# Optimization experiments

Measured on AMD Instinct MI355X. Metric: run time of the kernel, lower is better.

Reference implementation:

```python
import jax, jax.numpy as jnp
import numpy as np

INCH, OUTCH, H, W = 1536, 256, 60, 60
B = 4


def resize_bilinear_align_corners(x, oh, ow):
    """F.interpolate(x, (oh, ow), mode='bilinear', align_corners=True) for NCHW x."""
    Bx, C, Hx, Wx = x.shape
    ys = jnp.linspace(0.0, Hx - 1.0, oh)
    xs = jnp.linspace(0.0, Wx - 1.0, ow)
    y0 = jnp.floor(ys).astype(jnp.int32)
    x0 = jnp.floor(xs).astype(jnp.int32)
    y1 = jnp.minimum(y0 + 1, Hx - 1)
    x1 = jnp.minimum(x0 + 1, Wx - 1)
    wy = (ys - y0.astype(x.dtype))[:, None]   # [oh,1]
    wx = (xs - x0.astype(x.dtype))[None, :]   # [1,ow]
    g = lambda yi, xi: x[:, :, yi][:, :, :, xi]  # [B,C,oh,ow]
    top = (1.0 - wx) * g(y0, x0) + wx * g(y0, x1)
    bot = (1.0 - wx) * g(y1, x0) + wx * g(y1, x1)
    return (1.0 - wy) * top + wy * bot


def setup_inputs() -> dict:
    key = jax.random.key(0)
    ks = jax.random.split(key, 8)
    feat_supp = jax.random.normal(ks[0], (B, INCH, H, W), dtype=jnp.float32)
    feat_query = jax.random.normal(ks[1], (B, INCH, H, W), dtype=jnp.float32)
    mask_supp = jax.random.uniform(ks[2], (B, 1, 473, 473), dtype=jnp.float32)
    scale = 0.02
    W_lpf = jax.random.normal(ks[3], (OUTCH, INCH), dtype=jnp.float32) * scale   # shared_LPF 1x1 conv
    W_supp = jax.random.normal(ks[4], (OUTCH, INCH), dtype=jnp.float32) * scale  # supp_linear
    W_query = jax.random.normal(ks[5], (OUTCH, INCH), dtype=jnp.float32) * scale # query_linear
    W_final = jax.random.normal(ks[6], (OUTCH, 2 * OUTCH), dtype=jnp.float32) * scale
    b_final = jax.random.normal(ks[7], (OUTCH,), dtype=jnp.float32) * scale
    return {"feat_supp": feat_supp, "feat_query": feat_query, "mask_supp": mask_supp,
            "W_lpf": W_lpf, "W_supp": W_supp, "W_query": W_query,
            "W_final": W_final, "b_final": b_final}


def conv1x1(x, Wm):
    # x: [b,c,h,w], Wm: [o,c]
    return jnp.einsum('bchw,oc->bohw', x, Wm)


def reference(feat_supp, feat_query, mask_supp, W_lpf, W_supp, W_query, W_final, b_final):
    b, d, h, w = feat_supp.shape
    hw = h * w
    v_supp = conv1x1(feat_supp, W_lpf)    # [b,256,h,w]
    v_query = conv1x1(feat_query, W_lpf)  # [b,256,h,w]
    k = conv1x1(feat_supp, W_supp).transpose(0, 2, 3, 1).reshape(b, hw, -1)   # [b,hw,256]
    q = conv1x1(feat_query, W_query).transpose(0, 2, 3, 1).reshape(b, hw, -1) # [b,hw,256]
    attn = jnp.einsum('bqd,bkd->bqk', q, k)  # [b,hw,hw]
    fg_mask = resize_bilinear_align_corners(mask_supp, h, w)  # [b,1,h,w]
    bg_suppress = ((1.0 - fg_mask) * -999.0).reshape(b, 1, hw)
    attn = jax.nn.softmax(attn + bg_suppress, axis=-1)
    vs = v_supp.transpose(0, 2, 3, 1).reshape(b, hw, -1)      # [b,hw,256]
    out = jnp.einsum('bqk,bkd->bqd', attn, vs)                # [b,hw,256]
    out = out.reshape(b, h, w, -1).transpose(0, 3, 1, 2)      # [b,256,h,w]
    cat = jnp.concatenate([out, v_query], axis=1)             # [b,512,h,w]
    final = jax.nn.relu(conv1x1(cat, W_final) + b_final[None, :, None, None])
    return final, attn.reshape(b, h, w, h, w)
```

## Files before the change

### kernel.cpp

```cpp
#include <hip/hip_runtime.h>
#include <stdint.h>

typedef unsigned short u16;
typedef _Float16 h16;
typedef __attribute__((ext_vector_type(4))) float f32x4;
typedef __attribute__((ext_vector_type(8))) short s16x8;
typedef __attribute__((ext_vector_type(8))) _Float16 h16x8;
typedef __attribute__((ext_vector_type(4))) _Float16 h16x4;
typedef __attribute__((ext_vector_type(4))) unsigned short u16x4;
typedef __attribute__((ext_vector_type(8))) unsigned short u16x8;

#define HW   3600
#define HWP  3648
#define DIM  256
#define CIN  1536
#define LDK  72
#define NCB  58
#define PSH  15.0f

__device__ __forceinline__ u16 f2bf(float f) {
  uint32_t u = __float_as_uint(f);
  uint32_t r = (u + 0x7fffu + ((u >> 16) & 1u)) >> 16;
  return (u16)r;
}
__device__ __forceinline__ float bf2f(u16 h) { return __uint_as_float((uint32_t)h << 16); }

template<int MR, int NR>
__device__ __forceinline__ void mfma_tile(const h16 (*As)[LDK], const h16 (*Bs)[LDK],
                                          int lane, int wr, int wc, f32x4 acc[MR][NR]) {
#pragma unroll
  for (int ks = 0; ks < 2; ++ks) {
    const int ko = ks * 32 + ((lane >> 4) << 3);
    h16x8 af[MR], bv[NR];
#pragma unroll
    for (int m = 0; m < MR; ++m) af[m] = *(const h16x8*)&As[wr + m * 16 + (lane & 15)][ko];
#pragma unroll
    for (int n = 0; n < NR; ++n) bv[n] = *(const h16x8*)&Bs[wc + n * 16 + (lane & 15)][ko];
#pragma unroll
    for (int m = 0; m < MR; ++m)
#pragma unroll
      for (int n = 0; n < NR; ++n)
        acc[m][n] = __builtin_amdgcn_mfma_f32_16x16x32_f16(af[m], bv[n], acc[m][n], 0, 0, 0);
  }
}

template<int MR, int NR>
__device__ __forceinline__ void mfma_tile_bf(const u16 (*As)[LDK], const u16 (*Bs)[LDK],
                                             int lane, int wr, int wc, f32x4 acc[MR][NR]) {
#pragma unroll
  for (int ks = 0; ks < 2; ++ks) {
    const int ko = ks * 32 + ((lane >> 4) << 3);
    s16x8 af[MR], bv[NR];
#pragma unroll
    for (int m = 0; m < MR; ++m) af[m] = *(const s16x8*)&As[wr + m * 16 + (lane & 15)][ko];
#pragma unroll
    for (int n = 0; n < NR; ++n) bv[n] = *(const s16x8*)&Bs[wc + n * 16 + (lane & 15)][ko];
#pragma unroll
    for (int m = 0; m < MR; ++m)
#pragma unroll
      for (int n = 0; n < NR; ++n)
        acc[m][n] = __builtin_amdgcn_mfma_f32_16x16x32_bf16(af[m], bv[n], acc[m][n], 0, 0, 0);
  }
}

#define NW    (256 * 1536)
#define NWF   (256 * 512)
#define NPAD  (4 * 256 * 48)
#define NPREP (14400 + 3 * NW + NWF + NPAD)

__global__ __launch_bounds__(256) void k_prep(
    const float* __restrict__ mask, const float* __restrict__ Wlpf,
    const float* __restrict__ Wsupp, const float* __restrict__ Wquery,
    const float* __restrict__ Wfin,
    float* __restrict__ sup, h16* __restrict__ Wl16, h16* __restrict__ Ws16,
    h16* __restrict__ Wq16, h16* __restrict__ Wf16, u16* __restrict__ vs) {
  int i = blockIdx.x * 256 + threadIdx.x;
  if (i < 14400) {
    int b = i / HW, p = i % HW, py = p / 60, px = p % 60;
    float fg = mask[(size_t)b * 473 * 473 + (size_t)(py * 8) * 473 + px * 8];
    sup[i] = (1.0f - fg) * -999.0f;
  } else if (i < 14400 + NW) {
    int j = i - 14400; Wl16[j] = (h16)Wlpf[j];
  } else if (i < 14400 + 2 * NW) {
    int j = i - 14400 - NW; Ws16[j] = (h16)Wsupp[j];
  } else if (i < 14400 + 3 * NW) {
    int j = i - 14400 - 2 * NW; Wq16[j] = (h16)Wquery[j];
  } else if (i < 14400 + 3 * NW + NWF) {
    int j = i - 14400 - 3 * NW; Wf16[j] = (h16)Wfin[j];
  } else if (i < NPREP) {
    int j = i - 14400 - 3 * NW - NWF;
    int b = j / (256 * 48), rem = j % (256 * 48), d = rem / 48, kk = rem % 48;
    vs[((size_t)b * DIM + d) * HWP + 3600 + kk] = 0;
  }
}

__global__ __launch_bounds__(512, 4) void k_conv(
    const h16* __restrict__ Wl16, const h16* __restrict__ Ws16, const h16* __restrict__ Wq16,
    const float* __restrict__ featS, const float* __restrict__ featQ,
    u16* __restrict__ vs, h16* __restrict__ vq,
    h16* __restrict__ kbuf, h16* __restrict__ qbuf) {
  const int lin = blockIdx.x;
  const int xcd = lin & 7, slot = lin >> 3;
  const int ct = slot >> 1, rb = slot & 1;
  const int b = xcd & 3, isQ = xcd >> 2;
  const int colBase = ct * 128;
  const int tid = threadIdx.x, lane = tid & 63, wid = tid >> 6;
  const int wr = (wid >> 1) << 6, wc = (wid & 1) << 6;
  const h16* Wsel = (rb == 0) ? Wl16 : (isQ ? Wq16 : Ws16);
  const float* feat = (isQ ? featQ : featS) + (size_t)b * CIN * HW;

  __shared__ h16 As[256][LDK];
  __shared__ h16 Bs[128][LDK];
  f32x4 acc[4][4] = {};

  const int a_r = tid >> 3, a_kv = (tid & 7) << 3;
  const int b_px = (tid & 31) << 2;
  const int b_kb = (tid >> 5) << 2;
  const int gpx0 = colBase + b_px;
  const int gpx = (gpx0 + 3 < HW) ? gpx0 : HW - 4;

  s16x8 aR[4];
  f32x4 bV[4];
#pragma unroll
  for (int i = 0; i < 4; ++i)
    aR[i] = *(const s16x8*)&Wsel[(size_t)(a_r + i * 64) * CIN + a_kv];
#pragma unroll
  for (int i = 0; i < 4; ++i)
    bV[i] = *(const f32x4*)&feat[(size_t)(b_kb + i) * HW + gpx];

  for (int kt = 0; kt < 24; ++kt) {
#pragma unroll
    for (int i = 0; i < 4; ++i) *(s16x8*)&As[a_r + i * 64][a_kv] = aR[i];
#pragma unroll
    for (int c = 0; c < 4; ++c) {
      h16x4 h = {(h16)bV[0][c], (h16)bV[1][c], (h16)bV[2][c], (h16)bV[3][c]};
      *(h16x4*)&Bs[b_px + c][b_kb] = h;
    }
    if (kt < 23) {
      const int k0n = (kt + 1) * 64;
#pragma unroll
      for (int i = 0; i < 4; ++i)
        aR[i] = *(const s16x8*)&Wsel[(size_t)(a_r + i * 64) * CIN + k0n + a_kv];
#pragma unroll
      for (int i = 0; i < 4; ++i)
        bV[i] = *(const f32x4*)&feat[(size_t)(k0n + b_kb + i) * HW + gpx];
    }
    __syncthreads();
    mfma_tile<4, 4>(As, Bs, lane, wr, wc, acc);
    __syncthreads();
  }

  if (rb == 0 && !isQ) {
    u16* dst = vs + (size_t)b * DIM * HWP;
#pragma unroll
    for (int m = 0; m < 4; ++m) {
      const int d0 = wr + m * 16 + ((lane >> 4) << 2);
#pragma unroll
      for (int n = 0; n < 4; ++n) {
        const int pix = colBase + wc + n * 16 + (lane & 15);
        if (pix < HW) {
#pragma unroll
          for (int r = 0; r < 4; ++r) dst[(size_t)(d0 + r) * HWP + pix] = f2bf(acc[m][n][r]);
        }
      }
    }
  } else {
    h16* dst = ((rb == 0) ? vq : (isQ ? qbuf : kbuf)) + (size_t)b * HW * DIM;
#pragma unroll
    for (int m = 0; m < 4; ++m) {
      const int d0 = wr + m * 16 + ((lane >> 4) << 2);
#pragma unroll
      for (int n = 0; n < 4; ++n) {
        const int pix = colBase + wc + n * 16 + (lane & 15);
        if (pix < HW) {
          h16x4 h = {(h16)acc[m][n][0], (h16)acc[m][n][1],
                     (h16)acc[m][n][2], (h16)acc[m][n][3]};
          *(h16x4*)&dst[(size_t)pix * DIM + d0] = h;
        }
      }
    }
  }
}

__global__ __launch_bounds__(256) void k_qk(
    const h16* __restrict__ qbuf, const h16* __restrict__ kbuf,
    const float* __restrict__ sup, u16* __restrict__ p, float* __restrict__ stat) {
  const int hwid = blockIdx.x;
  const int xcd = hwid & 7, pos = hwid >> 3;
  const int logical = (xcd < 4) ? xcd * 421 + pos : 1684 + (xcd - 4) * 420 + pos;
  const int b = logical / 841, rem = logical % 841;
  const int rt = rem / 29, ct = rem % 29;
  const int rowBase = rt * 128, colBase = ct * 128;
  const int tid = threadIdx.x, lane = tid & 63, wid = tid >> 6;
  const int wr = (wid >> 1) << 6, wc = (wid & 1) << 6;
  const h16* Aq = qbuf + (size_t)b * HW * DIM;
  const h16* Bk = kbuf + (size_t)b * HW * DIM;

  __shared__ __align__(16) char smem[128 * LDK * 2 * 2];
  h16 (*As)[LDK] = (h16(*)[LDK])smem;
  h16 (*Bs)[LDK] = (h16(*)[LDK])(smem + 128 * LDK * 2);
  u16 (*pC)[136] = (u16(*)[136])smem;

  f32x4 acc[4][4] = {};
  const int r0 = tid >> 3, kv8 = (tid & 7) << 3;

  int gaR[4], gbR[4];
#pragma unroll
  for (int i = 0; i < 4; ++i) {
    const int r = r0 + i * 32;
    int ga = rowBase + r; gaR[i] = ga < HW ? ga : HW - 1;
    int gb = colBase + r; gbR[i] = gb < HW ? gb : HW - 1;
  }
  s16x8 aR[4], bR[4];
#pragma unroll
  for (int i = 0; i < 4; ++i) {
    aR[i] = *(const s16x8*)(Aq + (size_t)gaR[i] * DIM + kv8);
    bR[i] = *(const s16x8*)(Bk + (size_t)gbR[i] * DIM + kv8);
  }

  for (int kt = 0; kt < 4; ++kt) {
#pragma unroll
    for (int i = 0; i < 4; ++i) {
      *(s16x8*)&As[r0 + i * 32][kv8] = aR[i];
      *(s16x8*)&Bs[r0 + i * 32][kv8] = bR[i];
    }
    if (kt < 3) {
      const int k0n = (kt + 1) * 64;
#pragma unroll
      for (int i = 0; i < 4; ++i) {
        aR[i] = *(const s16x8*)(Aq + (size_t)gaR[i] * DIM + k0n + kv8);
        bR[i] = *(const s16x8*)(Bk + (size_t)gbR[i] * DIM + k0n + kv8);
      }
    }
    __syncthreads();
    mfma_tile<4, 4>(As, Bs, lane, wr, wc, acc);
    __syncthreads();
  }

  float sup4[4]; int kp4[4];
#pragma unroll
  for (int n = 0; n < 4; ++n) {
    const int kp = colBase + wc + n * 16 + (lane & 15);
    kp4[n] = kp;
    sup4[n] = (kp < HW) ? sup[b * HW + kp] : 0.f;
  }
  float* st = stat + (size_t)(b * NCB + ct * 2 + (wc >> 6)) * HW;
#pragma unroll
  for (int m = 0; m < 4; ++m) {
#pragma unroll
    for (int r = 0; r < 4; ++r) {
      float pr[4];
      float ls = 0.f;
#pragma unroll
      for (int n = 0; n < 4; ++n) {
        pr[n] = (kp4[n] < HW) ? __expf(acc[m][n][r] + sup4[n] - PSH) : 0.f;
        ls += pr[n];
      }
#pragma unroll
      for (int off = 1; off < 16; off <<= 1) ls += __shfl_xor(ls, off);
      const int rl = wr + m * 16 + ((lane >> 4) << 2) + r;
      if ((lane & 15) == 0) {
        const int qp = rowBase + rl;
        if (qp < HW) st[qp] = ls;
      }
#pragma unroll
      for (int n = 0; n < 4; ++n) pC[rl][wc + n * 16 + (lane & 15)] = f2bf(pr[n]);
    }
  }
  __syncthreads();
  u16* pB = p + (size_t)b * HW * HWP;
#pragma unroll
  for (int pass = 0; pass < 8; ++pass) {
    const int rl = pass * 16 + (tid >> 4);
    const int qp = rowBase + rl;
    const int col = colBase + (tid & 15) * 8;
    if (qp < HW && col < HW) {
      u16x8 v = *(const u16x8*)&pC[rl][(tid & 15) * 8];
      *(u16x8*)&pB[(size_t)qp * HWP + col] = v;
    }
  }
}

__global__ __launch_bounds__(256) void k_rowsum(const float* __restrict__ stat,
                                                float* __restrict__ invS) {
  const int i = blockIdx.x * 256 + threadIdx.x;
  if (i >= 4 * HW) return;
  const int b = i / HW, row = i % HW;
  const float* s = stat + (size_t)b * NCB * HW + row;
  float S = 0.f;
  for (int c = 0; c < NCB; ++c) S += s[(size_t)c * HW];
  invS[i] = 1.0f / S;
}

__global__ __launch_bounds__(256) void k_pvsm(
    const u16* __restrict__ p, const u16* __restrict__ vs,
    const float* __restrict__ invS, float* __restrict__ attn, float* __restrict__ part) {
  const int lin = blockIdx.x;
  const int xcd = lin & 7, slot = lin >> 3;
  const int b = xcd >> 1, sphalf = xcd & 1;
  const int split = sphalf * 2 + (slot & 1);
  const int rt = slot >> 1;
  const int rowBase = rt * 64;
  const int tid = threadIdx.x, lane = tid & 63, wid = tid >> 6;
  const int wc = wid << 6;
  const u16* pB = p + (size_t)b * HW * HWP;
  const u16* Bv = vs + (size_t)b * DIM * HWP;
  float* Ab = attn + (size_t)b * HW * HW;

  __shared__ u16 As[64][LDK];
  __shared__ u16 Bs[256][LDK];
  __shared__ float Ir[64];
  f32x4 acc[4][4] = {};

  if (tid < 64) {
    const int ga = rowBase + tid;
    Ir[tid] = (ga < HW) ? invS[b * HW + ga] : 0.f;
  }
  __syncthreads();

  const int a_r = tid >> 4, a_kv = (tid & 15) << 2;
  const int b_r = tid >> 3, b_kv = (tid & 7) << 3;
  const int t0 = split * 15, t1 = (split == 3) ? 57 : split * 15 + 15;

  u16x4 pR[4];
  s16x8 vR[8];
  {
    const int kc = t0 * 64 + a_kv;
#pragma unroll
    for (int i = 0; i < 4; ++i) {
      const int ga = rowBase + a_r + i * 16;
      pR[i] = (u16x4){0, 0, 0, 0};
      if (ga < HW && kc < HW) pR[i] = *(const u16x4*)&pB[(size_t)ga * HWP + kc];
    }
#pragma unroll
    for (int i = 0; i < 8; ++i)
      vR[i] = *(const s16x8*)&Bv[(size_t)(b_r + i * 32) * HWP + t0 * 64 + b_kv];
  }

  for (int kt = t0; kt < t1; ++kt) {
    const int kc = kt * 64 + a_kv;
#pragma unroll
    for (int i = 0; i < 4; ++i) {
      const int r = a_r + i * 16;
      const int ga = rowBase + r;
      if (ga < HW && kc < HW) {
        const float I = Ir[r];
        f32x4 w;
#pragma unroll
        for (int c = 0; c < 4; ++c) w[c] = bf2f(pR[i][c]) * I;
        __builtin_nontemporal_store(w, (f32x4*)(Ab + (size_t)ga * HW + kc));
      }
      *(u16x4*)&As[r][a_kv] = pR[i];
    }
#pragma unroll
    for (int i = 0; i < 8; ++i) *(s16x8*)&Bs[b_r + i * 32][b_kv] = vR[i];
    if (kt + 1 < t1) {
      const int kcn = (kt + 1) * 64 + a_kv;
#pragma unroll
      for (int i = 0; i < 4; ++i) {
        const int ga = rowBase + a_r + i * 16;
        pR[i] = (u16x4){0, 0, 0, 0};
        if (ga < HW && kcn < HW) pR[i] = *(const u16x4*)&pB[(size_t)ga * HWP + kcn];
      }
#pragma unroll
      for (int i = 0; i < 8; ++i)
        vR[i] = *(const s16x8*)&Bv[(size_t)(b_r + i * 32) * HWP + (kt + 1) * 64 + b_kv];
    }
    __syncthreads();
    mfma_tile_bf<4, 4>(As, Bs, lane, 0, wc, acc);
    __syncthreads();
  }
  float* dst = part + (size_t)(split * 4 + b) * HW * DIM;
#pragma unroll
  for (int m = 0; m < 4; ++m) {
    const int pix0 = rowBase + m * 16 + ((lane >> 4) << 2);
#pragma unroll
    for (int n = 0; n < 4; ++n) {
      const int d = wc + n * 16 + (lane & 15);
#pragma unroll
      for (int r = 0; r < 4; ++r)
        if (pix0 + r < HW) dst[(size_t)(pix0 + r) * DIM + d] = acc[m][n][r];
    }
  }
}

__global__ __launch_bounds__(256) void k_final(
    const float* __restrict__ part, const h16* __restrict__ vq,
    const h16* __restrict__ Wf16, const float* __restrict__ bfin,
    const float* __restrict__ invS, float* __restrict__ outF) {
  const int tid = threadIdx.x, lane = tid & 63, wid = tid >> 6;
  const int wr = (wid >> 1) << 5, wc = (wid & 1) << 6;
  const int rowBase = blockIdx.x * 64;
  const int colBase = blockIdx.y * 128;
  const int b = blockIdx.z;
  const h16* Avq = vq + (size_t)b * HW * DIM;
  const size_t pstride = (size_t)4 * HW * DIM;

  __shared__ h16 As[64][LDK];
  __shared__ h16 Bs[128][LDK];
  f32x4 acc[2][4] = {};

  const int a_r = tid >> 3, a_kv = (tid & 7) << 3;
  int gaR[2]; float IrT[2];
#pragma unroll
  for (int i = 0; i < 2; ++i) {
    int ga = rowBase + a_r + i * 32; gaR[i] = ga < HW ? ga : HW - 1;
    IrT[i] = invS[b * HW + gaR[i]];
  }

  s16x8 aR[2], bR[4];
#pragma unroll
  for (int i = 0; i < 2; ++i) {
    const float* pb = part + ((size_t)b * HW + gaR[i]) * DIM + a_kv;
    f32x4 s0 = *(const f32x4*)pb, s1 = *(const f32x4*)(pb + 4);
#pragma unroll
    for (int sp = 1; sp < 4; ++sp) {
      s0 += *(const f32x4*)(pb + sp * pstride);
      s1 += *(const f32x4*)(pb + sp * pstride + 4);
    }
    h16x8 h;
#pragma unroll
    for (int c = 0; c < 4; ++c) { h[c] = (h16)(s0[c] * IrT[i]); h[4 + c] = (h16)(s1[c] * IrT[i]); }
    aR[i] = *(s16x8*)&h;
  }
#pragma unroll
  for (int i = 0; i < 4; ++i)
    bR[i] = *(const s16x8*)(Wf16 + (size_t)(colBase + a_r + i * 32) * 512 + a_kv);

  for (int kt = 0; kt < 8; ++kt) {
#pragma unroll
    for (int i = 0; i < 2; ++i) *(s16x8*)&As[a_r + i * 32][a_kv] = aR[i];
#pragma unroll
    for (int i = 0; i < 4; ++i) *(s16x8*)&Bs[a_r + i * 32][a_kv] = bR[i];
    if (kt < 7) {
      const int k0n = (kt + 1) * 64;
      if (k0n < 256) {
#pragma unroll
        for (int i = 0; i < 2; ++i) {
          const float* pb = part + ((size_t)b * HW + gaR[i]) * DIM + k0n + a_kv;
          f32x4 s0 = *(const f32x4*)pb, s1 = *(const f32x4*)(pb + 4);
#pragma unroll
          for (int sp = 1; sp < 4; ++sp) {
            s0 += *(const f32x4*)(pb + sp * pstride);
            s1 += *(const f32x4*)(pb + sp * pstride + 4);
          }
          h16x8 h;
#pragma unroll
          for (int c = 0; c < 4; ++c) { h[c] = (h16)(s0[c] * IrT[i]); h[4 + c] = (h16)(s1[c] * IrT[i]); }
          aR[i] = *(s16x8*)&h;
        }
      } else {
        const int ak = k0n - 256;
#pragma unroll
        for (int i = 0; i < 2; ++i)
          aR[i] = *(const s16x8*)(Avq + (size_t)gaR[i] * DIM + ak + a_kv);
      }
#pragma unroll
      for (int i = 0; i < 4; ++i)
        bR[i] = *(const s16x8*)(Wf16 + (size_t)(colBase + a_r + i * 32) * 512 + k0n + a_kv);
    }
    __syncthreads();
    mfma_tile<2, 4>(As, Bs, lane, wr, wc, acc);
    __syncthreads();
  }
  float* dst = outF + (size_t)b * DIM * HW;
#pragma unroll
  for (int n = 0; n < 4; ++n) {
    const int o = colBase + wc + n * 16 + (lane & 15);
    const float bb = bfin[o];
#pragma unroll
    for (int m = 0; m < 2; ++m) {
      const int pix0 = rowBase + wr + m * 16 + ((lane >> 4) << 2);
      if (pix0 < HW) {
        f32x4 v;
#pragma unroll
        for (int r = 0; r < 4; ++r) v[r] = fmaxf(acc[m][n][r] + bb, 0.f);
        *(f32x4*)(dst + (size_t)o * HW + pix0) = v;
      }
    }
  }
}

extern "C" void kernel_launch(void* const* d_in, const int* in_sizes, int n_in,
                              void* d_out, int out_size, void* d_ws, size_t ws_size,
                              hipStream_t stream) {
  (void)in_sizes; (void)n_in; (void)out_size; (void)ws_size;
  const float* featS  = (const float*)d_in[0];
  const float* featQ  = (const float*)d_in[1];
  const float* mask   = (const float*)d_in[2];
  const float* Wlpf   = (const float*)d_in[3];
  const float* Wsupp  = (const float*)d_in[4];
  const float* Wquery = (const float*)d_in[5];
  const float* Wfin   = (const float*)d_in[6];
  const float* bfin   = (const float*)d_in[7];

  float* outF = (float*)d_out;
  float* attn = outF + (size_t)4 * DIM * HW;

  char* w = (char*)d_ws;
  h16* qbuf = (h16*)w;  w += (size_t)4 * HW * DIM * 2;
  h16* kbuf = (h16*)w;  w += (size_t)4 * HW * DIM * 2;
  u16* vs   = (u16*)w;  w += (size_t)4 * DIM * HWP * 2;
  h16* vq   = (h16*)w;  w += (size_t)4 * HW * DIM * 2;
  float* part = (float*)w;  w += (size_t)4 * 4 * HW * DIM * 4;
  u16* pbuf = (u16*)w;  w += (size_t)4 * HW * HWP * 2;
  h16* Wl16 = (h16*)w;  w += (size_t)NW * 2;
  h16* Ws16 = (h16*)w;  w += (size_t)NW * 2;
  h16* Wq16 = (h16*)w;  w += (size_t)NW * 2;
  h16* Wf16 = (h16*)w;  w += (size_t)NWF * 2;
  float* stat = (float*)w;  w += (size_t)4 * NCB * HW * 4;
  float* invS = (float*)w;  w += (size_t)4 * HW * 4;
  float* sup  = (float*)w;

  k_prep<<<dim3((NPREP + 255) / 256), 256, 0, stream>>>(
      mask, Wlpf, Wsupp, Wquery, Wfin, sup, Wl16, Ws16, Wq16, Wf16, vs);
  k_conv<<<dim3(464), 512, 0, stream>>>(Wl16, Ws16, Wq16, featS, featQ,
                                        vs, vq, kbuf, qbuf);
  k_qk<<<dim3(3364), 256, 0, stream>>>(qbuf, kbuf, sup, pbuf, stat);
  k_rowsum<<<dim3(57), 256, 0, stream>>>(stat, invS);
  k_pvsm<<<dim3(912), 256, 0, stream>>>(pbuf, vs, invS, attn, part);
  k_final<<<dim3(57, 2, 4), 256, 0, stream>>>(part, vq, Wf16, bfin, invS, outF);
}
```

Baseline: 271.8 us.

## Load conv weights directly to LDS and move barriers before prefetch loads

The conv kernel now streams weight tiles from global memory straight into an unpadded LDS buffer with global_load_lds, issued after the compute barrier. This drops the register staging and ds_write for that operand. In all four GEMM kernels the first barrier now sits right after the LDS stores and before the next-tile prefetch, so the global loads are in flight while the MFMA tile runs. The changes risk LDS bank conflicts from the unpadded 64-wide A layout, and need correct vmcnt waits so the direct LDS writes finish before the next barrier.

```diff
diff --git a/kernel.cpp b/kernel.cpp
--- a/kernel.cpp
+++ b/kernel.cpp
@@ -25,6 +25,11 @@
 }
 __device__ __forceinline__ float bf2f(u16 h) { return __uint_as_float((uint32_t)h << 16); }
 
+__device__ __forceinline__ void gload16(const void* g, void* l) {
+  __builtin_amdgcn_global_load_lds((const __attribute__((address_space(1))) void*)g,
+                                   (__attribute__((address_space(3))) void*)l, 16, 0, 0);
+}
+
 template<int MR, int NR>
 __device__ __forceinline__ void mfma_tile(const h16 (*As)[LDK], const h16 (*Bs)[LDK],
                                           int lane, int wr, int wc, f32x4 acc[MR][NR]) {
@@ -40,6 +45,24 @@
     for (int m = 0; m < MR; ++m)
 #pragma unroll
       for (int n = 0; n < NR; ++n)
+        acc[m][n] = __builtin_amdgcn_mfma_f32_16x16x32_f16(af[m], bv[n], acc[m][n], 0, 0, 0);
+  }
+}
+
+__device__ __forceinline__ void mfma_conv(const h16 (*As)[64], const h16 (*Bs)[LDK],
+                                          int lane, int wr, int wc, f32x4 acc[4][4]) {
+#pragma unroll
+  for (int ks = 0; ks < 2; ++ks) {
+    const int ko = ks * 32 + ((lane >> 4) << 3);
+    h16x8 af[4], bv[4];
+#pragma unroll
+    for (int m = 0; m < 4; ++m) af[m] = *(const h16x8*)&As[wr + m * 16 + (lane & 15)][ko];
+#pragma unroll
+    for (int n = 0; n < 4; ++n) bv[n] = *(const h16x8*)&Bs[wc + n * 16 + (lane & 15)][ko];
+#pragma unroll
+    for (int m = 0; m < 4; ++m)
+#pragma unroll
+      for (int n = 0; n < 4; ++n)
         acc[m][n] = __builtin_amdgcn_mfma_f32_16x16x32_f16(af[m], bv[n], acc[m][n], 0, 0, 0);
   }
 }
@@ -109,45 +132,47 @@
   const h16* Wsel = (rb == 0) ? Wl16 : (isQ ? Wq16 : Ws16);
   const float* feat = (isQ ? featQ : featS) + (size_t)b * CIN * HW;
 
-  __shared__ h16 As[256][LDK];
+  __shared__ h16 As[256][64];
   __shared__ h16 Bs[128][LDK];
   f32x4 acc[4][4] = {};
 
-  const int a_r = tid >> 3, a_kv = (tid & 7) << 3;
   const int b_px = (tid & 31) << 2;
   const int b_kb = (tid >> 5) << 2;
   const int gpx0 = colBase + b_px;
   const int gpx = (gpx0 + 3 < HW) ? gpx0 : HW - 4;
 
-  s16x8 aR[4];
+  const h16* aSrc = Wsel + (size_t)(wid * 32 + (lane >> 3)) * CIN + (lane & 7) * 8;
+  h16* aDst = &As[wid * 32][0];
+
   f32x4 bV[4];
 #pragma unroll
   for (int i = 0; i < 4; ++i)
-    aR[i] = *(const s16x8*)&Wsel[(size_t)(a_r + i * 64) * CIN + a_kv];
+    gload16(aSrc + (size_t)(i * 8) * CIN, aDst + i * 512);
 #pragma unroll
   for (int i = 0; i < 4; ++i)
     bV[i] = *(const f32x4*)&feat[(size_t)(b_kb + i) * HW + gpx];
 
   for (int kt = 0; kt < 24; ++kt) {
-#pragma unroll
-    for (int i = 0; i < 4; ++i) *(s16x8*)&As[a_r + i * 64][a_kv] = aR[i];
 #pragma unroll
     for (int c = 0; c < 4; ++c) {
       h16x4 h = {(h16)bV[0][c], (h16)bV[1][c], (h16)bV[2][c], (h16)bV[3][c]};
       *(h16x4*)&Bs[b_px + c][b_kb] = h;
     }
+    __syncthreads();
     if (kt < 23) {
       const int k0n = (kt + 1) * 64;
 #pragma unroll
       for (int i = 0; i < 4; ++i)
-        aR[i] = *(const s16x8*)&Wsel[(size_t)(a_r + i * 64) * CIN + k0n + a_kv];
+        bV[i] = *(const f32x4*)&feat[(size_t)(k0n + b_kb + i) * HW + gpx];
+    }
+    mfma_conv(As, Bs, lane, wr, wc, acc);
+    __syncthreads();
+    if (kt < 23) {
+      const int k0n = (kt + 1) * 64;
 #pragma unroll
       for (int i = 0; i < 4; ++i)
-        bV[i] = *(const f32x4*)&feat[(size_t)(k0n + b_kb + i) * HW + gpx];
-    }
-    __syncthreads();
-    mfma_tile<4, 4>(As, Bs, lane, wr, wc, acc);
-    __syncthreads();
+        gload16(aSrc + (size_t)(i * 8) * CIN + k0n, aDst + i * 512);
+    }
   }
 
   if (rb == 0 && !isQ) {
@@ -224,6 +249,7 @@
       *(s16x8*)&As[r0 + i * 32][kv8] = aR[i];
       *(s16x8*)&Bs[r0 + i * 32][kv8] = bR[i];
     }
+    __syncthreads();
     if (kt < 3) {
       const int k0n = (kt + 1) * 64;
 #pragma unroll
@@ -232,7 +258,6 @@
         bR[i] = *(const s16x8*)(Bk + (size_t)gbR[i] * DIM + k0n + kv8);
       }
     }
-    __syncthreads();
     mfma_tile<4, 4>(As, Bs, lane, wr, wc, acc);
     __syncthreads();
   }
@@ -354,6 +379,7 @@
     }
 #pragma unroll
     for (int i = 0; i < 8; ++i) *(s16x8*)&Bs[b_r + i * 32][b_kv] = vR[i];
+    __syncthreads();
     if (kt + 1 < t1) {
       const int kcn = (kt + 1) * 64 + a_kv;
 #pragma unroll
@@ -366,7 +392,6 @@
       for (int i = 0; i < 8; ++i)
         vR[i] = *(const s16x8*)&Bv[(size_t)(b_r + i * 32) * HWP + (kt + 1) * 64 + b_kv];
     }
-    __syncthreads();
     mfma_tile_bf<4, 4>(As, Bs, lane, 0, wc, acc);
     __syncthreads();
   }
@@ -432,6 +457,7 @@
     for (int i = 0; i < 2; ++i) *(s16x8*)&As[a_r + i * 32][a_kv] = aR[i];
 #pragma unroll
     for (int i = 0; i < 4; ++i) *(s16x8*)&Bs[a_r + i * 32][a_kv] = bR[i];
+    __syncthreads();
     if (kt < 7) {
       const int k0n = (kt + 1) * 64;
       if (k0n < 256) {
@@ -459,7 +485,6 @@
       for (int i = 0; i < 4; ++i)
         bR[i] = *(const s16x8*)(Wf16 + (size_t)(colBase + a_r + i * 32) * 512 + k0n + a_kv);
     }
-    __syncthreads();
     mfma_tile<2, 4>(As, Bs, lane, wr, wc, acc);
     __syncthreads();
   }
```

After: 276.9 us. Within noise of the previous version (+1.9%).
